# Optimization experiments

Measured on AMD Instinct MI355X. Metric: run time of the kernel, lower is better.

## Reference

```python
import jax, jax.numpy as jnp
import numpy as np
import math

DIM = 1024
EPS = 1e-6

def rms_norm(x):
    return x * jax.lax.rsqrt(jnp.mean(x * x, axis=-1, keepdims=True) + EPS)

def setup_inputs() -> dict:
    key = jax.random.key(0)
    k1, k2, k3 = jax.random.split(key, 3)
    T, B, D = 512, 32, DIM
    x = jax.random.normal(k1, (T, B, D), dtype=jnp.float32)
    h0 = jnp.zeros((B, D), dtype=jnp.float32)
    # Parameters: W xavier-uniform, W_h ~ orthogonal-ish scaled by 0.01, b zeros
    bound = math.sqrt(6.0 / (D + D))
    W = jax.random.uniform(k2, (D, D), minval=-bound, maxval=bound, dtype=jnp.float32)
    W_h = 0.01 * jax.random.normal(k3, (D, D), dtype=jnp.float32) / math.sqrt(D)
    b = jnp.zeros((D,), dtype=jnp.float32)
    log_alpha = jnp.asarray(math.log(0.1), dtype=jnp.float32)
    log_beta = jnp.asarray(math.log(0.01), dtype=jnp.float32)
    return {"x": x, "h0": h0, "W": W, "W_h": W_h, "b": b,
            "log_alpha": log_alpha, "log_beta": log_beta}

def reference(x, h0, W, W_h, b, log_alpha, log_beta):
    alpha = jnp.exp(log_alpha)
    beta = jax.nn.sigmoid(log_beta) * 0.1
    # Precompute input projection for all timesteps: [T,B,D]
    Wx_all = jnp.einsum('tbd,ed->tbe', x, W) + b

    def step(h_prev, wx_t):
        h_new = h_prev + alpha * wx_t + beta * (h_prev @ W_h.T)
        h_new = rms_norm(h_new)
        out = h_new * jax.nn.silu(h_new)
        return h_new, (h_new, out)

    _, (hs, outs) = jax.lax.scan(step, h0, Wx_all)
    h = jnp.concatenate([h0[None], hs], axis=0)  # [T+1,B,D]
    return outs, h
```

## Files before the change

### kernel.cpp

```cpp
#include <hip/hip_runtime.h>
#include <stdint.h>

#define T_STEPS 512
#define BATCH   32
#define DIMN    1024
#define MROWS   (T_STEPS*BATCH)
#define BD      (BATCH*DIMN)

typedef _Float16 f16;
typedef _Float16 f16x8 __attribute__((ext_vector_type(8)));
typedef _Float16 f16x2 __attribute__((ext_vector_type(2)));
typedef float    f32x4 __attribute__((ext_vector_type(4)));

union U8 { f16x8 v; f16x2 p[4]; };

__device__ __forceinline__ f16x2 pkrtz(float a, float b) {
  return __builtin_bit_cast(f16x2, __builtin_amdgcn_cvt_pkrtz(a, b));
}

__device__ __forceinline__ void load16_to_lds(const f16* gptr, f16* lptr) {
  __builtin_amdgcn_global_load_lds(
      (const __attribute__((address_space(1))) unsigned int*)(uintptr_t)gptr,
      (__attribute__((address_space(3))) unsigned int*)(uint32_t)(uintptr_t)lptr,
      16, 0, 0);
}

template<int CTRL>
__device__ __forceinline__ float dpp_ror_add(float v) {
  int iv = __float_as_int(v);
  int rv = __builtin_amdgcn_update_dpp(iv, iv, CTRL, 0xF, 0xF, false);
  return v + __int_as_float(rv);
}

__device__ __forceinline__ float wave_allsum(float s) {
  s = dpp_ror_add<0x128>(s);
  s = dpp_ror_add<0x124>(s);
  s = dpp_ror_add<0x122>(s);
  s = dpp_ror_add<0x121>(s);
  float a = __int_as_float(__builtin_amdgcn_readlane(__float_as_int(s), 0));
  float b = __int_as_float(__builtin_amdgcn_readlane(__float_as_int(s), 16));
  float c = __int_as_float(__builtin_amdgcn_readlane(__float_as_int(s), 32));
  float d = __int_as_float(__builtin_amdgcn_readlane(__float_as_int(s), 48));
  return (a + b) + (c + d);
}

__global__ __launch_bounds__(256) void cvt_f32_f16(const float* __restrict__ src,
                                                   f16* __restrict__ dst, int n8) {
  int i = blockIdx.x * 256 + threadIdx.x;
  if (i >= n8) return;
  const float4* s = (const float4*)src;
  float4 a = s[2*i], b = s[2*i + 1];
  f16x8 o = { (f16)a.x, (f16)a.y, (f16)a.z, (f16)a.w,
              (f16)b.x, (f16)b.y, (f16)b.z, (f16)b.w };
  *(f16x8*)(dst + (size_t)i * 8) = o;
}

__global__ __launch_bounds__(256) void gemm_bt_f16(
    const f16* __restrict__ A, const f16* __restrict__ B,
    const float* __restrict__ bias, f16* __restrict__ Cout,
    const float* __restrict__ la, const float* __restrict__ lb,
    const float* __restrict__ rowscale, const f16* __restrict__ addend, int mode) {
  constexpr int K = DIMN;
  constexpr int N = DIMN;
  __shared__ f16 Alds[128 * 32];
  __shared__ f16 Blds[128 * 32];
  const int tid  = threadIdx.x;
  const int lane = tid & 63;
  const int wid  = tid >> 6;
  const int wm = wid & 1, wn = wid >> 1;
  const int l15  = lane & 15;
  const int quad = lane >> 4;
  const int swz  = (l15 >> 1) & 3;
  const int rowBase = blockIdx.x * 128;
  const int colBase = blockIdx.y * 128;
  const int sr = lane >> 2;
  const int cs = lane & 3;

  const float scale = (mode == 0) ? expf(la[0])
                                  : 0.1f / (1.0f + expf(-lb[0]));

  f32x4 acc[4][4] = {};

  for (int k0 = 0; k0 < K; k0 += 32) {
    #pragma unroll
    for (int i = 0; i < 2; ++i) {
      const int g = wid + i * 4;
      const int r = g * 16 + sr;
      const int cd = cs ^ ((r >> 1) & 3);
      load16_to_lds(A + (size_t)(rowBase + r) * K + k0 + cd * 8, Alds + g * 512);
      load16_to_lds(B + (size_t)(colBase + r) * K + k0 + cd * 8, Blds + g * 512);
    }
    __syncthreads();
    f16x8 af[4], bf[4];
    #pragma unroll
    for (int mi = 0; mi < 4; ++mi) {
      const int r = wm * 64 + mi * 16 + l15;
      af[mi] = *(const f16x8*)(Alds + r * 32 + (quad ^ swz) * 8);
    }
    #pragma unroll
    for (int ni = 0; ni < 4; ++ni) {
      const int r = wn * 64 + ni * 16 + l15;
      bf[ni] = *(const f16x8*)(Blds + r * 32 + (quad ^ swz) * 8);
    }
    #pragma unroll
    for (int mi = 0; mi < 4; ++mi)
      #pragma unroll
      for (int ni = 0; ni < 4; ++ni)
        acc[mi][ni] = __builtin_amdgcn_mfma_f32_16x16x32_f16(af[mi], bf[ni], acc[mi][ni], 0, 0, 0);
    __syncthreads();
  }

  float colb[4];
  #pragma unroll
  for (int ni = 0; ni < 4; ++ni)
    colb[ni] = (mode == 0) ? bias[colBase + wn * 64 + ni * 16 + l15] : 0.0f;

  #pragma unroll
  for (int mi = 0; mi < 4; ++mi) {
    const int m0 = rowBase + wm * 64 + mi * 16 + quad * 4;
    #pragma unroll
    for (int j = 0; j < 4; ++j) {
      const size_t row = (size_t)(m0 + j);
      const float rs = (mode == 0)
          ? scale
          : scale * rowscale[(((int)row & 31) << 9) | ((int)row >> 5)];
      #pragma unroll
      for (int ni = 0; ni < 4; ++ni) {
        const int n = colBase + wn * 64 + ni * 16 + l15;
        float v;
        if (mode == 0) v = rs * (acc[mi][ni][j] + colb[ni]);
        else           v = fmaf(rs, acc[mi][ni][j], (float)addend[row * N + n]);
        Cout[row * N + n] = (f16)v;
      }
    }
  }
}

__global__ __launch_bounds__(256) void gram_f16(
    const f16* __restrict__ A, f16* __restrict__ Gout) {
  const int bx = blockIdx.x, by = blockIdx.y, bz = blockIdx.z;
  if (by < bx) return;
  __shared__ f16 Alds[128 * 32];
  __shared__ f16 Blds[128 * 32];
  const int tid  = threadIdx.x;
  const int lane = tid & 63;
  const int wid  = tid >> 6;
  const int wm = wid & 1, wn = wid >> 1;
  const int l15  = lane & 15;
  const int quad = lane >> 4;
  const int swz  = (l15 >> 1) & 3;
  const int rowBase = bx * 128;
  const int colBase = by * 128;
  const int sr = lane >> 2;
  const int cs = lane & 3;
  const f16* Ab = A + (size_t)bz * DIMN;

  f32x4 acc[4][4] = {};

  for (int k0 = 0; k0 < DIMN; k0 += 32) {
    #pragma unroll
    for (int i = 0; i < 2; ++i) {
      const int g = wid + i * 4;
      const int r = g * 16 + sr;
      const int cd = cs ^ ((r >> 1) & 3);
      load16_to_lds(Ab + (size_t)(rowBase + r) * BD + k0 + cd * 8, Alds + g * 512);
      load16_to_lds(Ab + (size_t)(colBase + r) * BD + k0 + cd * 8, Blds + g * 512);
    }
    __syncthreads();
    f16x8 af[4], bf[4];
    #pragma unroll
    for (int mi = 0; mi < 4; ++mi) {
      const int r = wm * 64 + mi * 16 + l15;
      af[mi] = *(const f16x8*)(Alds + r * 32 + (quad ^ swz) * 8);
    }
    #pragma unroll
    for (int ni = 0; ni < 4; ++ni) {
      const int r = wn * 64 + ni * 16 + l15;
      bf[ni] = *(const f16x8*)(Blds + r * 32 + (quad ^ swz) * 8);
    }
    #pragma unroll
    for (int mi = 0; mi < 4; ++mi)
      #pragma unroll
      for (int ni = 0; ni < 4; ++ni)
        acc[mi][ni] = __builtin_amdgcn_mfma_f32_16x16x32_f16(af[mi], bf[ni], acc[mi][ni], 0, 0, 0);
    __syncthreads();
  }

  f16* Gb = Gout + (size_t)bz * (T_STEPS * T_STEPS);
  #pragma unroll
  for (int mi = 0; mi < 4; ++mi) {
    const int m0 = rowBase + wm * 64 + mi * 16 + quad * 4;
    #pragma unroll
    for (int j = 0; j < 4; ++j) {
      #pragma unroll
      for (int ni = 0; ni < 4; ++ni) {
        const int n = colBase + wn * 64 + ni * 16 + l15;
        Gb[(size_t)(m0 + j) * T_STEPS + n] = (f16)acc[mi][ni][j];
      }
    }
  }
}

__global__ __launch_bounds__(256) void gemv_p(
    const f16* __restrict__ Wm, const float* __restrict__ h0,
    float* __restrict__ P) {
  const int b = blockIdx.x, sg = blockIdx.y;
  const int w = threadIdx.x >> 6, l = threadIdx.x & 63;
  float h[16];
  {
    const float* hp = h0 + (size_t)b * DIMN + l * 16;
    #pragma unroll
    for (int i = 0; i < 4; ++i) {
      float4 a = *(const float4*)(hp + i * 4);
      h[i*4+0] = a.x; h[i*4+1] = a.y; h[i*4+2] = a.z; h[i*4+3] = a.w;
    }
  }
  for (int k = 0; k < 16; ++k) {
    const int s = sg * 64 + w * 16 + k;
    const f16* wp = Wm + (size_t)s * BD + (size_t)b * DIMN + l * 16;
    f16x8 a0 = *(const f16x8*)(wp);
    f16x8 a1 = *(const f16x8*)(wp + 8);
    float acc = 0.f;
    #pragma unroll
    for (int i = 0; i < 8; ++i) acc = fmaf((float)a0[i], h[i], acc);
    #pragma unroll
    for (int i = 0; i < 8; ++i) acc = fmaf((float)a1[i], h[i+8], acc);
    acc = wave_allsum(acc);
    if (l == 0) P[(size_t)b * 512 + s] = acc;
  }
}

template<int SHIFT>
__global__ __launch_bounds__(64, 1) void scalar_scan(
    const f16* __restrict__ Gm, const float* __restrict__ P,
    const float* __restrict__ h0,
    float* __restrict__ Carr, float* __restrict__ Sarr) {
  const int b = blockIdx.x, l = threadIdx.x;
  const f16* Gb = Gm + (size_t)b * (T_STEPS * T_STEPS);
  float N;
  {
    const float* hp = h0 + (size_t)b * DIMN + l * 16;
    float na = 0.f;
    #pragma unroll
    for (int i = 0; i < 4; ++i) {
      float4 a = *(const float4*)(hp + i * 4);
      na = fmaf(a.x, a.x, na); na = fmaf(a.y, a.y, na);
      na = fmaf(a.z, a.z, na); na = fmaf(a.w, a.w, na);
    }
    N = wave_allsum(na);
  }
  float d[8];
  {
    float4 p0 = *(const float4*)(P + (size_t)b * 512 + l * 8);
    float4 p1 = *(const float4*)(P + (size_t)b * 512 + l * 8 + 4);
    d[0]=p0.x; d[1]=p0.y; d[2]=p0.z; d[3]=p0.w;
    d[4]=p1.x; d[5]=p1.y; d[6]=p1.z; d[7]=p1.w;
  }
  float gd[8];
  #pragma unroll
  for (int j = 0; j < 8; ++j)
    gd[j] = (float)Gb[(size_t)(l * 8 + j) * T_STEPS + (l * 8 + j)];
  f16x8 grow[8];
  #pragma unroll
  for (int j = 0; j < 8; ++j)
    grow[j] = *(const f16x8*)(Gb + (size_t)j * T_STEPS + l * 8);

  float c = 1.f, ic = 1.f, kk = 1.f / DIMN;
  if (SHIFT && l == 0) Sarr[(size_t)b * 512] = 1.f;
  float ccap = 1.f, iccap = 1.f;

  for (int tb = 0; tb < T_STEPS; tb += 8) {
    const int a = tb >> 3;
    #pragma unroll
    for (int J = 0; J < 8; ++J) {
      const int t = tb + J;
      f16x8 g = grow[J];
      int tn = t + 8; if (tn > T_STEPS - 1) tn = T_STEPS - 1;
      grow[J] = *(const f16x8*)(Gb + (size_t)tn * T_STEPS + l * 8);
      const float e   = __int_as_float(__builtin_amdgcn_readlane(__float_as_int(d[J]),  a));
      const float gtt = __int_as_float(__builtin_amdgcn_readlane(__float_as_int(gd[J]), a));
      const float cold = c;
      #pragma unroll
      for (int j2 = 0; j2 < 8; ++j2) d[j2] = fmaf(cold, (float)g[j2], d[j2]);
      N = fmaf(2.f * cold, e, fmaf(cold * cold, gtt, N));
      const float m   = fmaf(N, kk, 1e-6f);
      const float rho = __builtin_amdgcn_rsqf(m);
      c  = cold * (m * rho);
      ic = ic * rho;
      kk = kk * (rho * rho);
      ccap  = (l == J) ? cold : ccap;
      iccap = (l == J) ? ic   : iccap;
    }
    if (l < 8) {
      Carr[(size_t)b * 512 + tb + l] = ccap;
      const int sidx = tb + SHIFT + l;
      if (sidx < T_STEPS) Sarr[(size_t)b * 512 + sidx] = iccap;
    }
  }
}

__global__ __launch_bounds__(64) void recombine0(
    const f16* __restrict__ Wx, const float* __restrict__ h0,
    const float* __restrict__ Carr, f16* __restrict__ G0) {
  const int b = blockIdx.x, dc = blockIdx.y, l = threadIdx.x;
  const size_t base = (size_t)b * DIMN + dc * 128 + l * 2;
  float u0 = h0[base], u1 = h0[base + 1];
  *(f16x2*)(G0 + base) = pkrtz(u0, u1);
  f16x2 wbuf[8];
  #pragma unroll
  for (int j = 0; j < 8; ++j) wbuf[j] = *(const f16x2*)(Wx + (size_t)j * BD + base);
  const float* Cb = Carr + (size_t)b * 512;
  for (int tb = 0; tb < T_STEPS; tb += 8) {
    float4 ca = *(const float4*)(Cb + tb);
    float4 cz = *(const float4*)(Cb + tb + 4);
    const float cc[8] = {ca.x, ca.y, ca.z, ca.w, cz.x, cz.y, cz.z, cz.w};
    #pragma unroll
    for (int J = 0; J < 8; ++J) {
      const int t = tb + J;
      f16x2 w = wbuf[J];
      int tn = t + 8; if (tn > T_STEPS - 1) tn = T_STEPS - 1;
      wbuf[J] = *(const f16x2*)(Wx + (size_t)tn * BD + base);
      u0 = fmaf(cc[J], (float)w[0], u0);
      u1 = fmaf(cc[J], (float)w[1], u1);
      if (t < T_STEPS - 1)
        *(f16x2*)(G0 + (size_t)(t + 1) * BD + base) = pkrtz(u0, u1);
    }
  }
}

__global__ __launch_bounds__(64) void recombine1_expand(
    const f16* __restrict__ Cin, const float* __restrict__ h0,
    const float* __restrict__ Carr, const float* __restrict__ Sarr,
    float* __restrict__ outs, float* __restrict__ hout) {
  const int b = blockIdx.x, dc = blockIdx.y, l = threadIdx.x;
  if (dc == 8) {
    const size_t o = (size_t)b * DIMN + (size_t)l * 16;
    #pragma unroll
    for (int i = 0; i < 4; ++i) {
      float4 a = *(const float4*)(h0 + o + i * 4);
      *(float4*)(hout + o + i * 4) = a;
    }
    return;
  }
  const size_t base = (size_t)b * DIMN + dc * 128 + l * 2;
  float u0 = h0[base], u1 = h0[base + 1];
  f16x2 wbuf[8];
  #pragma unroll
  for (int j = 0; j < 8; ++j) wbuf[j] = *(const f16x2*)(Cin + (size_t)j * BD + base);
  const float* Cb = Carr + (size_t)b * 512;
  const float* Sb = Sarr + (size_t)b * 512;
  for (int tb = 0; tb < T_STEPS; tb += 8) {
    float4 ca = *(const float4*)(Cb + tb);
    float4 cz = *(const float4*)(Cb + tb + 4);
    float4 sa = *(const float4*)(Sb + tb);
    float4 sz = *(const float4*)(Sb + tb + 4);
    const float cc[8] = {ca.x, ca.y, ca.z, ca.w, cz.x, cz.y, cz.z, cz.w};
    const float ss[8] = {sa.x, sa.y, sa.z, sa.w, sz.x, sz.y, sz.z, sz.w};
    #pragma unroll
    for (int J = 0; J < 8; ++J) {
      const int t = tb + J;
      f16x2 w = wbuf[J];
      int tn = t + 8; if (tn > T_STEPS - 1) tn = T_STEPS - 1;
      wbuf[J] = *(const f16x2*)(Cin + (size_t)tn * BD + base);
      u0 = fmaf(cc[J], (float)w[0], u0);
      u1 = fmaf(cc[J], (float)w[1], u1);
      const float v0 = ss[J] * u0, v1 = ss[J] * u1;
      const float o0 = v0 * v0 / (1.f + expf(-v0));
      const float o1 = v1 * v1 / (1.f + expf(-v1));
      *(float2*)(outs + (size_t)t * BD + base) = make_float2(o0, o1);
      *(float2*)(hout + (size_t)(t + 1) * BD + base) = make_float2(v0, v1);
    }
  }
}

extern "C" void kernel_launch(void* const* d_in, const int* in_sizes, int n_in,
                              void* d_out, int out_size, void* d_ws, size_t ws_size,
                              hipStream_t stream) {
  const float* x    = (const float*)d_in[0];
  const float* h0   = (const float*)d_in[1];
  const float* W    = (const float*)d_in[2];
  const float* Wh   = (const float*)d_in[3];
  const float* bias = (const float*)d_in[4];
  const float* la   = (const float*)d_in[5];
  const float* lb   = (const float*)d_in[6];

  char* ws = (char*)d_ws;
  f16* XH   = (f16*)(ws);
  f16* GRAM = (f16*)(ws);
  f16* W16  = (f16*)(ws + 33554432ull);
  f16* WH16 = (f16*)(ws + 35651584ull);
  f16* WX16 = (f16*)(ws + 37748736ull);
  f16* G0   = (f16*)(ws + 71303168ull);
  f16* C16  = (f16*)(ws + 104857600ull);
  float* S0 = (float*)(ws + 33554432ull);
  float* C0 = (float*)(ws + 33554432ull + 65536ull);
  float* P0 = (float*)(ws + 33554432ull + 131072ull);
  float* S1 = (float*)(ws + 35651584ull);
  float* C1 = (float*)(ws + 35651584ull + 65536ull);
  float* P1 = (float*)(ws + 35651584ull + 131072ull);

  float* outs = (float*)d_out;
  float* hout = outs + (size_t)T_STEPS * BD;

  cvt_f32_f16<<<dim3((MROWS * DIMN / 8) / 256), 256, 0, stream>>>(x, XH, MROWS * DIMN / 8);
  cvt_f32_f16<<<dim3((DIMN * DIMN / 8) / 256), 256, 0, stream>>>(W, W16, DIMN * DIMN / 8);
  cvt_f32_f16<<<dim3((DIMN * DIMN / 8) / 256), 256, 0, stream>>>(Wh, WH16, DIMN * DIMN / 8);

  gemm_bt_f16<<<dim3(MROWS / 128, DIMN / 128), 256, 0, stream>>>(
      XH, W16, bias, WX16, la, lb, nullptr, nullptr, 0);

  gram_f16<<<dim3(4, 4, BATCH), 256, 0, stream>>>(WX16, GRAM);
  gemv_p<<<dim3(BATCH, 8), 256, 0, stream>>>(WX16, h0, P0);
  scalar_scan<1><<<dim3(BATCH), 64, 0, stream>>>(GRAM, P0, h0, C0, S0);
  recombine0<<<dim3(BATCH, 8), 64, 0, stream>>>(WX16, h0, C0, G0);

  gemm_bt_f16<<<dim3(MROWS / 128, DIMN / 128), 256, 0, stream>>>(
      G0, WH16, nullptr, C16, la, lb, S0, WX16, 1);

  gram_f16<<<dim3(4, 4, BATCH), 256, 0, stream>>>(C16, GRAM);
  gemv_p<<<dim3(BATCH, 8), 256, 0, stream>>>(C16, h0, P1);
  scalar_scan<0><<<dim3(BATCH), 64, 0, stream>>>(GRAM, P1, h0, C1, S1);
  recombine1_expand<<<dim3(BATCH, 9), 64, 0, stream>>>(C16, h0, C1, S1, outs, hout);
}
```

Measured before the change: 626.1 us.

## Parallelize recombine prefix-sums over time chunks with two-pass chunked scan

Replaces the sequential per-column time scan in the recombine kernels (256 blocks of 64 threads walking all 512 steps) with a two-pass chunked scan. A chunk_partial kernel computes per-64-step partial sums, and the recombine kernels then add the prefix of earlier partials and scan only their own chunk across 8 time chunks. Each thread also handles 4 columns with f16x4 loads and float4 stores. This multiplies the available parallelism to fill the GPU, at the cost of an extra pass reading the input and a small partials buffer.

```diff
diff --git a/kernel.cpp b/kernel.cpp
--- a/kernel.cpp
+++ b/kernel.cpp
@@ -9,10 +9,12 @@
 
 typedef _Float16 f16;
 typedef _Float16 f16x8 __attribute__((ext_vector_type(8)));
+typedef _Float16 f16x4 __attribute__((ext_vector_type(4)));
 typedef _Float16 f16x2 __attribute__((ext_vector_type(2)));
 typedef float    f32x4 __attribute__((ext_vector_type(4)));
 
 union U8 { f16x8 v; f16x2 p[4]; };
+union U4 { f16x4 v; f16x2 p[2]; };
 
 __device__ __forceinline__ f16x2 pkrtz(float a, float b) {
   return __builtin_bit_cast(f16x2, __builtin_amdgcn_cvt_pkrtz(a, b));
@@ -299,76 +301,133 @@
   }
 }
 
-__global__ __launch_bounds__(64) void recombine0(
+__global__ __launch_bounds__(64) void chunk_partial(
+    const f16* __restrict__ Win, const float* __restrict__ Carr,
+    float* __restrict__ PS) {
+  const int b = blockIdx.x, dcy = blockIdx.y, tc = blockIdx.z;
+  const int l = threadIdx.x;
+  const size_t base = (size_t)b * DIMN + dcy * 256 + l * 4;
+  const float* Cb = Carr + (size_t)b * 512;
+  const int t0 = tc * 64;
+  float a0 = 0.f, a1 = 0.f, a2 = 0.f, a3 = 0.f;
+  f16x4 ring[8];
+  #pragma unroll
+  for (int j = 0; j < 8; ++j)
+    ring[j] = *(const f16x4*)(Win + (size_t)(t0 + j) * BD + base);
+  for (int tt = 0; tt < 64; tt += 8) {
+    float4 ca = *(const float4*)(Cb + t0 + tt);
+    float4 cz = *(const float4*)(Cb + t0 + tt + 4);
+    const float cc[8] = {ca.x, ca.y, ca.z, ca.w, cz.x, cz.y, cz.z, cz.w};
+    #pragma unroll
+    for (int J = 0; J < 8; ++J) {
+      f16x4 w = ring[J];
+      int tn = t0 + tt + J + 8; if (tn > T_STEPS - 1) tn = T_STEPS - 1;
+      ring[J] = *(const f16x4*)(Win + (size_t)tn * BD + base);
+      a0 = fmaf(cc[J], (float)w[0], a0);
+      a1 = fmaf(cc[J], (float)w[1], a1);
+      a2 = fmaf(cc[J], (float)w[2], a2);
+      a3 = fmaf(cc[J], (float)w[3], a3);
+    }
+  }
+  *(float4*)(PS + (size_t)tc * BD + base) = make_float4(a0, a1, a2, a3);
+}
+
+__global__ __launch_bounds__(64) void recomb0B(
     const f16* __restrict__ Wx, const float* __restrict__ h0,
-    const float* __restrict__ Carr, f16* __restrict__ G0) {
-  const int b = blockIdx.x, dc = blockIdx.y, l = threadIdx.x;
-  const size_t base = (size_t)b * DIMN + dc * 128 + l * 2;
-  float u0 = h0[base], u1 = h0[base + 1];
-  *(f16x2*)(G0 + base) = pkrtz(u0, u1);
-  f16x2 wbuf[8];
-  #pragma unroll
-  for (int j = 0; j < 8; ++j) wbuf[j] = *(const f16x2*)(Wx + (size_t)j * BD + base);
+    const float* __restrict__ Carr, const float* __restrict__ PS,
+    f16* __restrict__ G0) {
+  const int b = blockIdx.x, dcy = blockIdx.y, tc = blockIdx.z;
+  const int l = threadIdx.x;
+  const size_t base = (size_t)b * DIMN + dcy * 256 + l * 4;
+  float4 h = *(const float4*)(h0 + base);
+  float u0 = h.x, u1 = h.y, u2 = h.z, u3 = h.w;
+  for (int p = 0; p < tc; ++p) {
+    float4 ps = *(const float4*)(PS + (size_t)p * BD + base);
+    u0 += ps.x; u1 += ps.y; u2 += ps.z; u3 += ps.w;
+  }
+  if (tc == 0) {
+    U4 g; g.p[0] = pkrtz(u0, u1); g.p[1] = pkrtz(u2, u3);
+    *(f16x4*)(G0 + base) = g.v;
+  }
   const float* Cb = Carr + (size_t)b * 512;
-  for (int tb = 0; tb < T_STEPS; tb += 8) {
-    float4 ca = *(const float4*)(Cb + tb);
-    float4 cz = *(const float4*)(Cb + tb + 4);
+  const int t0 = tc * 64;
+  f16x4 ring[8];
+  #pragma unroll
+  for (int j = 0; j < 8; ++j)
+    ring[j] = *(const f16x4*)(Wx + (size_t)(t0 + j) * BD + base);
+  for (int tt = 0; tt < 64; tt += 8) {
+    float4 ca = *(const float4*)(Cb + t0 + tt);
+    float4 cz = *(const float4*)(Cb + t0 + tt + 4);
     const float cc[8] = {ca.x, ca.y, ca.z, ca.w, cz.x, cz.y, cz.z, cz.w};
     #pragma unroll
     for (int J = 0; J < 8; ++J) {
-      const int t = tb + J;
-      f16x2 w = wbuf[J];
+      const int t = t0 + tt + J;
+      f16x4 w = ring[J];
       int tn = t + 8; if (tn > T_STEPS - 1) tn = T_STEPS - 1;
-      wbuf[J] = *(const f16x2*)(Wx + (size_t)tn * BD + base);
+      ring[J] = *(const f16x4*)(Wx + (size_t)tn * BD + base);
       u0 = fmaf(cc[J], (float)w[0], u0);
       u1 = fmaf(cc[J], (float)w[1], u1);
-      if (t < T_STEPS - 1)
-        *(f16x2*)(G0 + (size_t)(t + 1) * BD + base) = pkrtz(u0, u1);
-    }
-  }
-}
-
-__global__ __launch_bounds__(64) void recombine1_expand(
+      u2 = fmaf(cc[J], (float)w[2], u2);
+      u3 = fmaf(cc[J], (float)w[3], u3);
+      if (t < T_STEPS - 1) {
+        U4 g; g.p[0] = pkrtz(u0, u1); g.p[1] = pkrtz(u2, u3);
+        *(f16x4*)(G0 + (size_t)(t + 1) * BD + base) = g.v;
+      }
+    }
+  }
+}
+
+__global__ __launch_bounds__(64) void recomb1B(
     const f16* __restrict__ Cin, const float* __restrict__ h0,
     const float* __restrict__ Carr, const float* __restrict__ Sarr,
+    const float* __restrict__ PS,
     float* __restrict__ outs, float* __restrict__ hout) {
-  const int b = blockIdx.x, dc = blockIdx.y, l = threadIdx.x;
-  if (dc == 8) {
-    const size_t o = (size_t)b * DIMN + (size_t)l * 16;
-    #pragma unroll
-    for (int i = 0; i < 4; ++i) {
-      float4 a = *(const float4*)(h0 + o + i * 4);
-      *(float4*)(hout + o + i * 4) = a;
-    }
+  const int b = blockIdx.x, dcy = blockIdx.y, tc = blockIdx.z;
+  const int l = threadIdx.x;
+  const size_t base = (size_t)b * DIMN + dcy * 256 + l * 4;
+  if (tc == 8) {
+    float4 a = *(const float4*)(h0 + base);
+    *(float4*)(hout + base) = a;
     return;
   }
-  const size_t base = (size_t)b * DIMN + dc * 128 + l * 2;
-  float u0 = h0[base], u1 = h0[base + 1];
-  f16x2 wbuf[8];
-  #pragma unroll
-  for (int j = 0; j < 8; ++j) wbuf[j] = *(const f16x2*)(Cin + (size_t)j * BD + base);
+  float4 h = *(const float4*)(h0 + base);
+  float u0 = h.x, u1 = h.y, u2 = h.z, u3 = h.w;
+  for (int p = 0; p < tc; ++p) {
+    float4 ps = *(const float4*)(PS + (size_t)p * BD + base);
+    u0 += ps.x; u1 += ps.y; u2 += ps.z; u3 += ps.w;
+  }
   const float* Cb = Carr + (size_t)b * 512;
   const float* Sb = Sarr + (size_t)b * 512;
-  for (int tb = 0; tb < T_STEPS; tb += 8) {
-    float4 ca = *(const float4*)(Cb + tb);
-    float4 cz = *(const float4*)(Cb + tb + 4);
-    float4 sa = *(const float4*)(Sb + tb);
-    float4 sz = *(const float4*)(Sb + tb + 4);
+  const int t0 = tc * 64;
+  f16x4 ring[8];
+  #pragma unroll
+  for (int j = 0; j < 8; ++j)
+    ring[j] = *(const f16x4*)(Cin + (size_t)(t0 + j) * BD + base);
+  for (int tt = 0; tt < 64; tt += 8) {
+    float4 ca = *(const float4*)(Cb + t0 + tt);
+    float4 cz = *(const float4*)(Cb + t0 + tt + 4);
+    float4 sa = *(const float4*)(Sb + t0 + tt);
+    float4 sz = *(const float4*)(Sb + t0 + tt + 4);
     const float cc[8] = {ca.x, ca.y, ca.z, ca.w, cz.x, cz.y, cz.z, cz.w};
     const float ss[8] = {sa.x, sa.y, sa.z, sa.w, sz.x, sz.y, sz.z, sz.w};
     #pragma unroll
     for (int J = 0; J < 8; ++J) {
-      const int t = tb + J;
-      f16x2 w = wbuf[J];
+      const int t = t0 + tt + J;
+      f16x4 w = ring[J];
       int tn = t + 8; if (tn > T_STEPS - 1) tn = T_STEPS - 1;
-      wbuf[J] = *(const f16x2*)(Cin + (size_t)tn * BD + base);
+      ring[J] = *(const f16x4*)(Cin + (size_t)tn * BD + base);
       u0 = fmaf(cc[J], (float)w[0], u0);
       u1 = fmaf(cc[J], (float)w[1], u1);
+      u2 = fmaf(cc[J], (float)w[2], u2);
+      u3 = fmaf(cc[J], (float)w[3], u3);
       const float v0 = ss[J] * u0, v1 = ss[J] * u1;
+      const float v2 = ss[J] * u2, v3 = ss[J] * u3;
       const float o0 = v0 * v0 / (1.f + expf(-v0));
       const float o1 = v1 * v1 / (1.f + expf(-v1));
-      *(float2*)(outs + (size_t)t * BD + base) = make_float2(o0, o1);
-      *(float2*)(hout + (size_t)(t + 1) * BD + base) = make_float2(v0, v1);
+      const float o2 = v2 * v2 / (1.f + expf(-v2));
+      const float o3 = v3 * v3 / (1.f + expf(-v3));
+      *(float4*)(outs + (size_t)t * BD + base) = make_float4(o0, o1, o2, o3);
+      *(float4*)(hout + (size_t)(t + 1) * BD + base) = make_float4(v0, v1, v2, v3);
     }
   }
 }
@@ -392,12 +451,14 @@
   f16* WX16 = (f16*)(ws + 37748736ull);
   f16* G0   = (f16*)(ws + 71303168ull);
   f16* C16  = (f16*)(ws + 104857600ull);
-  float* S0 = (float*)(ws + 33554432ull);
-  float* C0 = (float*)(ws + 33554432ull + 65536ull);
-  float* P0 = (float*)(ws + 33554432ull + 131072ull);
-  float* S1 = (float*)(ws + 35651584ull);
-  float* C1 = (float*)(ws + 35651584ull + 65536ull);
-  float* P1 = (float*)(ws + 35651584ull + 131072ull);
+  float* S0  = (float*)(ws + 33554432ull);
+  float* C0  = (float*)(ws + 33554432ull + 65536ull);
+  float* P0  = (float*)(ws + 33554432ull + 131072ull);
+  float* PS0 = (float*)(ws + 33554432ull + 196608ull);
+  float* S1  = (float*)(ws + 35651584ull);
+  float* C1  = (float*)(ws + 35651584ull + 65536ull);
+  float* P1  = (float*)(ws + 35651584ull + 131072ull);
+  float* PS1 = (float*)(ws + 35651584ull + 196608ull);
 
   float* outs = (float*)d_out;
   float* hout = outs + (size_t)T_STEPS * BD;
@@ -412,7 +473,8 @@
   gram_f16<<<dim3(4, 4, BATCH), 256, 0, stream>>>(WX16, GRAM);
   gemv_p<<<dim3(BATCH, 8), 256, 0, stream>>>(WX16, h0, P0);
   scalar_scan<1><<<dim3(BATCH), 64, 0, stream>>>(GRAM, P0, h0, C0, S0);
-  recombine0<<<dim3(BATCH, 8), 64, 0, stream>>>(WX16, h0, C0, G0);
+  chunk_partial<<<dim3(BATCH, 4, 8), 64, 0, stream>>>(WX16, C0, PS0);
+  recomb0B<<<dim3(BATCH, 4, 8), 64, 0, stream>>>(WX16, h0, C0, PS0, G0);
 
   gemm_bt_f16<<<dim3(MROWS / 128, DIMN / 128), 256, 0, stream>>>(
       G0, WH16, nullptr, C16, la, lb, S0, WX16, 1);
@@ -420,5 +482,6 @@
   gram_f16<<<dim3(4, 4, BATCH), 256, 0, stream>>>(C16, GRAM);
   gemv_p<<<dim3(BATCH, 8), 256, 0, stream>>>(C16, h0, P1);
   scalar_scan<0><<<dim3(BATCH), 64, 0, stream>>>(GRAM, P1, h0, C1, S1);
-  recombine1_expand<<<dim3(BATCH, 9), 64, 0, stream>>>(C16, h0, C1, S1, outs, hout);
-}
+  chunk_partial<<<dim3(BATCH, 4, 8), 64, 0, stream>>>(C16, C1, PS1);
+  recomb1B<<<dim3(BATCH, 4, 9), 64, 0, stream>>>(C16, h0, C1, S1, PS1, outs, hout);
+}
```

New measurement: 572.9 us. -8.5%, faster.
